# Kernel tuning notes

Measured on AMD Instinct MI355X. Metric: run time of the kernel, lower is better.

Reference implementation:

```python
import jax, jax.numpy as jnp
import numpy as np

NUM_BLOCKS = 8
WIDTH = 512
HIDDEN_SIZE_FACTOR = 1
HARD_THRESH_FRAC = 1.0
BLOCK_SIZE = WIDTH // NUM_BLOCKS


def setup_inputs() -> dict:
    key = jax.random.key(0)
    k_x, k1, k2, k3, k4 = jax.random.split(key, 5)
    B, L, P, C = 4, 2048, WIDTH, 8
    bs = BLOCK_SIZE
    hf = HIDDEN_SIZE_FACTOR
    scale = 1.0 / (bs * bs * hf)
    x = jax.random.normal(k_x, (B, L, P, C), dtype=jnp.float32)
    w1 = scale * jax.random.uniform(k1, (2, NUM_BLOCKS, bs, bs * hf), dtype=jnp.float32)
    b1 = scale * jax.random.uniform(k2, (2, NUM_BLOCKS, bs * hf), dtype=jnp.float32)
    w2 = scale * jax.random.uniform(k3, (2, NUM_BLOCKS, bs * hf, bs), dtype=jnp.float32)
    b2 = scale * jax.random.uniform(k4, (2, NUM_BLOCKS, bs), dtype=jnp.float32)
    return {"x": x, "w1": w1, "b1": b1, "w2": w2, "b2": b2}


def _gelu(v):
    # torch nn.GELU default is the exact (erf) variant
    return jax.nn.gelu(v, approximate=False)


def reference(x, w1, b1, w2, b2):
    B, L, P, C = x.shape
    nb, bs = NUM_BLOCKS, BLOCK_SIZE
    # rfft along L (norm='ortho'); complex64
    xf = jnp.fft.rfft(x, axis=1, norm="ortho")          # (B, Lf, P, C)
    Lf = xf.shape[1]
    xf = jnp.transpose(xf, (0, 1, 3, 2))                  # (B, Lf, C, P)
    xf = xf.reshape(B, Lf, C, nb, bs)                     # split P into blocks
    kept = int(Lf * HARD_THRESH_FRAC)
    xr, xi = jnp.real(xf[:, :kept]), jnp.imag(xf[:, :kept])
    # block-diagonal complex 2-layer MLP
    mm = lambda a, w: jnp.einsum("blcni,nio->blcno", a, w)
    o1r = _gelu(mm(xr, w1[0]) - mm(xi, w1[1]) + b1[0])
    o1i = _gelu(mm(xi, w1[0]) + mm(xr, w1[1]) + b1[1])
    o2r = mm(o1r, w2[0]) - mm(o1i, w2[1]) + b2[0]
    o2i = mm(o1i, w2[0]) + mm(o1r, w2[1]) + b2[1]
    # zero-pad the thresholded modes (no-op when kept == Lf)
    pad = Lf - kept
    if pad > 0:
        z = jnp.zeros((B, pad, C, nb, bs), dtype=o2r.dtype)
        o2r = jnp.concatenate([o2r, z], axis=1)
        o2i = jnp.concatenate([o2i, z], axis=1)
    xc = (o2r + 1j * o2i).reshape(B, Lf, C, P)
    out = jnp.fft.irfft(xc, n=L, axis=1, norm="ortho")  # (B, L, C, P)
    out = jnp.transpose(out, (0, 1, 3, 2))               # (B, L, P, C)
    return (out + x).astype(x.dtype)
```

## Files before the change

### kernel.cpp

```cpp
#include <hip/hip_runtime.h>
#include <hip/hip_bf16.h>

typedef unsigned short u16;
typedef unsigned int   u32;
typedef __bf16 bf16x8 __attribute__((ext_vector_type(8)));
typedef float  f32x4  __attribute__((ext_vector_type(4)));
typedef u32    u32x2  __attribute__((ext_vector_type(2)));

#define KPAD 1088
#define PI_F 3.14159265358979323846f

__device__ __forceinline__ u16 f2bf(float f){
    u32 u = __float_as_uint(f);
    return (u16)((u + 0x7FFFu + ((u >> 16) & 1u)) >> 16);
}
__device__ __forceinline__ float bf2f(u16 v){ return __uint_as_float(((u32)v) << 16); }
__device__ __forceinline__ int zmap(int e){ return e + (e >> 4); }
__device__ __forceinline__ int brev10(int x){ return (int)(__brev((u32)x) >> 22); }

__global__ __launch_bounds__(256) void prep_w(const float* __restrict__ w1,
                                              const float* __restrict__ w2,
                                              u16* __restrict__ WSW){
    int gid = blockIdx.x * 256 + threadIdx.x;
    int qd = gid >> 12;
    int t  = qd & 1;
    int n  = (qd >> 1) & 7;
    int l  = qd >> 4;
    int rr = gid & 4095;
    int o  = rr >> 6;
    int k  = rr & 63;
    const float* w = l ? w2 : w1;
    WSW[gid] = f2bf(w[((size_t)(t*8 + n)*64 + k)*64 + o]);
}


__device__ __forceinline__ u16 unpack_one(const float2* Zc, int k, int pl, float sf){
    int rb  = zmap(brev10(k & 1023));
    int rmb = zmap(brev10((1024 - k) & 1023));
    float2 Zk = Zc[rb], Zm = Zc[rmb];
    float sn_, cs_; __sincosf(PI_F*(float)k*(1.0f/1024.0f), &sn_, &cs_);
    float Er=0.5f*(Zk.x+Zm.x), Ei=0.5f*(Zk.y-Zm.y);
    float Dr=0.5f*(Zk.x-Zm.x), Di=0.5f*(Zk.y+Zm.y);
    float Xr = Er + cs_*Di - sn_*Dr;
    float Xi = Ei - sn_*Di - cs_*Dr;
    return f2bf((pl ? Xi : Xr) * sf);
}

__global__ __launch_bounds__(256) void fwd_fft(const float* __restrict__ X,
                                               u16* __restrict__ S){
    __shared__ float2 Zs[4*1088];
    __shared__ float2 tws[544];
    int tid = threadIdx.x;
    int blk = blockIdx.x;
    int b = blk >> 10;
    int q = blk & 1023;
    int m8 = q & 7, tq = q >> 3;
    int Q = (tq >> 2)*8 + m8, s4 = tq & 3;
    int col0 = Q*16 + s4*4;
    int p  = col0 >> 3;
    int c0 = col0 & 7;
    int n  = p >> 6, pl_ = p & 63;

    for (int i = tid; i < 512; i += 256){
        float sv, cv; __sincosf(-2.0f*PI_F*(float)i*(1.0f/1024.0f), &sv, &cv);
        tws[zmap(i)] = make_float2(cv, sv);
    }
    for (int pi = tid; pi < 1024; pi += 256){
        size_t base = ((size_t)(b*2048 + 2*pi)*512 + p)*8 + c0;
        f32x4 ve = *(const f32x4*)(X + base);
        f32x4 vo = *(const f32x4*)(X + base + 4096);
        #pragma unroll
        for (int s = 0; s < 4; ++s)
            Zs[s*1088 + zmap(pi)] = make_float2(ve[s], vo[s]);
    }
    __syncthreads();
    for (int ms = 9; ms >= 0; --ms){
        int m = 1 << ms;
        for (int i = tid; i < 2048; i += 256){
            int s = i >> 9, bi = i & 511;
            int jj = bi & (m-1);
            int a  = ((bi >> ms) << (ms+1)) + jj;
            float2 u = Zs[s*1088 + zmap(a)];
            float2 v = Zs[s*1088 + zmap(a+m)];
            float2 w = tws[zmap(jj << (9-ms))];
            float dx = u.x - v.x, dy = u.y - v.y;
            Zs[s*1088 + zmap(a)]   = make_float2(u.x+v.x, u.y+v.y);
            Zs[s*1088 + zmap(a+m)] = make_float2(dx*w.x - dy*w.y, dx*w.y + dy*w.x);
        }
        __syncthreads();
    }
    const float sf = 0.02209708691207961f;
    int run = tid >> 5, tr = tid & 31;
    int ci = run >> 1, pl = run & 1;
    const float2* Zc = Zs + ci*1088;
    u16* rp = S + (size_t)((((b*8 + (c0+ci))*8 + n)*2 + pl)*64 + pl_)*KPAD;
    for (int kk = tr*2; kk <= 1024; kk += 64){
        u16 w0 = unpack_one(Zc, kk, pl, sf);
        if (kk < 1024){
            u16 w1 = unpack_one(Zc, kk+1, pl, sf);
            *(u32*)(rp + kk) = (u32)w0 | ((u32)w1 << 16);
        } else {
            rp[kk] = w0;
        }
    }
}

__device__ __forceinline__ bf16x8 fetchB(const u16* mat, int o64, int k64, bool neg){
    const u32x2* pb = (const u32x2*)(mat + o64*68 + k64);
    u32x2 lo = pb[0], hi = pb[1];
    union { u32 u[4]; bf16x8 v; } bt;
    bt.u[0]=lo.x; bt.u[1]=lo.y; bt.u[2]=hi.x; bt.u[3]=hi.y;
    if (neg){ bt.u[0]^=0x80008000u; bt.u[1]^=0x80008000u; bt.u[2]^=0x80008000u; bt.u[3]^=0x80008000u; }
    return bt.v;
}
__device__ __forceinline__ bf16x8 loadU16x8(const u16* pp){
    union { u32 u[4]; bf16x8 v; } t;
    const u32* qq = (const u32*)pp;
    t.u[0]=qq[0]; t.u[1]=qq[1]; t.u[2]=qq[2]; t.u[3]=qq[3];
    return t.v;
}

__global__ __launch_bounds__(256) void mlp_kernel(const u16* __restrict__ WSW,
                                                  const float* __restrict__ b1,
                                                  const float* __restrict__ b2,
                                                  u16* __restrict__ S){
    __shared__ __align__(16) u16 AT[4][64*68];
    __shared__ __align__(16) u16 AS[8448];
    int tid = threadIdx.x;
    int blk = blockIdx.x;
    int n = blk & 7;
    int rest = blk >> 3;
    int t17 = rest % 17;
    int bc  = rest / 17;
    int b = bc >> 3, c = bc & 7;
    int k0 = t17 << 6;
    int lane = tid & 63, wv = tid >> 6;
    int lane15 = lane & 15, quad = lane >> 4;

    for (int mi = 0; mi < 4; ++mi){
        const u32* src = (const u32*)(WSW + (size_t)(((mi>>1)*8 + n)*2 + (mi&1))*4096);
        u32* dstm = (u32*)AT[mi];
        for (int d = tid; d < 2048; d += 256){
            int o = d >> 5, kk2 = d & 31;
            dstm[o*34 + kk2] = src[d];
        }
    }
    float bb1[8], bb2v[8];
    #pragma unroll
    for (int nb = 0; nb < 8; ++nb){
        int col = nb*16 + lane15;
        int tt = col >> 6, cc = col & 63;
        bb1[nb]  = b1[tt*512 + n*64 + cc];
        bb2v[nb] = b2[tt*512 + n*64 + cc];
    }
    size_t SB = (size_t)(((b*8 + c)*8 + n)*2)*64;
    {
        int rsub = tid & 31;
        for (int rr = tid >> 5; rr < 128; rr += 8){
            const u16* rp = S + (SB + rr)*KPAD + k0;
            u32 w = *(const u32*)(rp + 2*rsub);
            AS[(2*rsub)*132 + rr]   = (u16)(w & 0xFFFFu);
            AS[(2*rsub+1)*132 + rr] = (u16)(w >> 16);
        }
    }
    __syncthreads();

    const u16* arow = AS + (wv*16 + lane15)*132;
    bf16x8 afr[4];
    #pragma unroll
    for (int kb = 0; kb < 4; ++kb)
        afr[kb] = loadU16x8(arow + kb*32 + quad*8);
    f32x4 acc[8];
    #pragma unroll
    for (int nb = 0; nb < 8; ++nb){ acc[nb][0]=bb1[nb]; acc[nb][1]=bb1[nb]; acc[nb][2]=bb1[nb]; acc[nb][3]=bb1[nb]; }
    #pragma unroll
    for (int nb = 0; nb < 8; ++nb){
        int o64 = (nb&3)*16 + lane15;
        #pragma unroll
        for (int kb = 0; kb < 4; ++kb){
            int k64 = (kb&1)*32 + quad*8;
            const u16* mat; bool neg = false;
            if (kb < 2) mat = (nb<4) ? AT[0] : AT[1];
            else { if (nb<4){ mat = AT[1]; neg = true; } else mat = AT[0]; }
            acc[nb] = __builtin_amdgcn_mfma_f32_16x16x32_bf16(afr[kb], fetchB(mat,o64,k64,neg), acc[nb], 0,0,0);
        }
    }
    #pragma unroll
    for (int nb = 0; nb < 8; ++nb){
        #pragma unroll
        for (int r4 = 0; r4 < 4; ++r4){
            float xv = acc[nb][r4];
            float u_ = xv * 0.70710678118f;
            float u2 = u_*u_;
            float pg = 1.0f + u2*(-0.333333333f + u2*(0.1f + u2*(-0.0238095238f)));
            float h  = 0.5f * xv * (1.0f + 1.12837916709551f * u_ * pg);
            AS[(wv*16 + quad*4 + r4)*132 + nb*16 + lane15] = f2bf(h);
        }
    }
    bf16x8 a2[4];
    #pragma unroll
    for (int kb = 0; kb < 4; ++kb)
        a2[kb] = loadU16x8(arow + kb*32 + quad*8);
    f32x4 acc2[8];
    #pragma unroll
    for (int nb = 0; nb < 8; ++nb){ acc2[nb][0]=bb2v[nb]; acc2[nb][1]=bb2v[nb]; acc2[nb][2]=bb2v[nb]; acc2[nb][3]=bb2v[nb]; }
    #pragma unroll
    for (int nb = 0; nb < 8; ++nb){
        int o64 = (nb&3)*16 + lane15;
        #pragma unroll
        for (int kb = 0; kb < 4; ++kb){
            int k64 = (kb&1)*32 + quad*8;
            const u16* mat; bool neg = false;
            if (kb < 2) mat = (nb<4) ? AT[2] : AT[3];
            else { if (nb<4){ mat = AT[3]; neg = true; } else mat = AT[2]; }
            acc2[nb] = __builtin_amdgcn_mfma_f32_16x16x32_bf16(a2[kb], fetchB(mat,o64,k64,neg), acc2[nb], 0,0,0);
        }
    }
    __syncthreads();
    #pragma unroll
    for (int nb = 0; nb < 8; ++nb){
        #pragma unroll
        for (int r4 = 0; r4 < 4; ++r4)
            AS[(nb*16 + lane15)*66 + (wv*16 + quad*4 + r4)] = f2bf(acc2[nb][r4]);
    }
    __syncthreads();
    {
        int rsub = tid & 31;
        int k = k0 + 2*rsub;
        for (int rr = tid >> 5; rr < 128; rr += 8){
            u32 val = *(const u32*)(AS + rr*66 + 2*rsub);
            u16* rp = S + (SB + rr)*KPAD + k0;
            if (k + 1 <= 1024)  *(u32*)(rp + 2*rsub) = val;
            else if (k == 1024) rp[2*rsub] = (u16)(val & 0xFFFFu);
        }
    }
}

__global__ __launch_bounds__(256) void inv_fft(const u16* __restrict__ S,
                                               const float* __restrict__ X,
                                               float* __restrict__ OUT){
    __shared__ float2 Zs[4*1088];
    __shared__ float2 tws[544];
    __shared__ float2 ysp[4];
    int tid = threadIdx.x;
    int blk = blockIdx.x;
    int b = blk >> 10;
    int q = blk & 1023;
    int m8 = q & 7, tq = q >> 3;
    int Q = (tq >> 2)*8 + m8, s4 = tq & 3;
    int col0 = Q*16 + s4*4;
    int p  = col0 >> 3;
    int c0 = col0 & 7;
    int n  = p >> 6, pl_ = p & 63;

    for (int i = tid; i < 512; i += 256){
        float sv, cv; __sincosf(-2.0f*PI_F*(float)i*(1.0f/1024.0f), &sv, &cv);
        tws[zmap(i)] = make_float2(cv, sv);
    }
    {
        int g = tid >> 6, l64 = tid & 63;
        const u16* rpR = S + (size_t)((((b*8 + (c0+g))*8 + n)*2 + 0)*64 + pl_)*KPAD;
        const u16* rpI = rpR + (size_t)64*KPAD;
        for (int kk = 2*l64; kk <= 1024; kk += 128){
            u32 wr = *(const u32*)(rpR + kk);
            u32 wi = *(const u32*)(rpI + kk);
            float yr0 = bf2f((u16)(wr & 0xFFFFu));
            float yi0 = bf2f((u16)(wi & 0xFFFFu));
            if (kk == 0)        Zs[g*1088 + zmap(0)] = make_float2(yr0, 0.0f);
            else if (kk == 1024) ysp[g] = make_float2(yr0, 0.0f);
            else                Zs[g*1088 + zmap(kk)] = make_float2(yr0, yi0);
            if (kk < 1024){
                float yr1 = bf2f((u16)(wr >> 16));
                float yi1 = bf2f((u16)(wi >> 16));
                Zs[g*1088 + zmap(kk+1)] = make_float2(yr1, yi1);
            }
        }
    }
    __syncthreads();
    for (int k = tid; k <= 512; k += 256){
        float s2_, c2_; __sincosf(PI_F*(float)k*(1.0f/1024.0f), &s2_, &c2_);
        #pragma unroll
        for (int s = 0; s < 4; ++s){
            float2 Yk = Zs[s*1088 + zmap(k)];
            float2 Ym = (k == 0) ? ysp[s] : Zs[s*1088 + zmap(1024 - k)];
            float Ex = 0.5f*(Yk.x + Ym.x);
            float Ey = 0.5f*(Yk.y - Ym.y);
            float Dx = 0.5f*(Yk.x - Ym.x);
            float Dy = 0.5f*(Yk.y + Ym.y);
            float Ox = c2_*Dx - s2_*Dy;
            float Oy = c2_*Dy + s2_*Dx;
            Zs[s*1088 + zmap(k)] = make_float2(Ex - Oy, Ey + Ox);
            if (k > 0 && k < 512)
                Zs[s*1088 + zmap(1024 - k)] = make_float2(Ex + Oy, Ox - Ey);
        }
    }
    __syncthreads();
    for (int ms = 9; ms >= 0; --ms){
        int m = 1 << ms;
        for (int i = tid; i < 2048; i += 256){
            int s = i >> 9, bi = i & 511;
            int jj = bi & (m-1);
            int a  = ((bi >> ms) << (ms+1)) + jj;
            float2 u = Zs[s*1088 + zmap(a)];
            float2 v = Zs[s*1088 + zmap(a+m)];
            float2 w = tws[zmap(jj << (9-ms))];
            float dx = u.x - v.x, dy = u.y - v.y;
            Zs[s*1088 + zmap(a)]   = make_float2(u.x+v.x, u.y+v.y);
            Zs[s*1088 + zmap(a+m)] = make_float2(dx*w.x - dy*w.y, dx*w.y + dy*w.x);
        }
        __syncthreads();
    }
    const float sc = 0.04419417382415922f;
    for (int pi = tid; pi < 1024; pi += 256){
        int f = (1024 - pi) & 1023;
        int zb = zmap(brev10(f));
        size_t base = ((size_t)(b*2048 + 2*pi)*512 + p)*8 + c0;
        f32x4 xe = *(const f32x4*)(X + base);
        f32x4 xo = *(const f32x4*)(X + base + 4096);
        f32x4 oe, oo;
        #pragma unroll
        for (int s = 0; s < 4; ++s){
            float2 r = Zs[s*1088 + zb];
            oe[s] = r.x*sc + xe[s];
            oo[s] = r.y*sc + xo[s];
        }
        *(f32x4*)(OUT + base)        = oe;
        *(f32x4*)(OUT + base + 4096) = oo;
    }
}

extern "C" void kernel_launch(void* const* d_in, const int* in_sizes, int n_in,
                              void* d_out, int out_size, void* d_ws, size_t ws_size,
                              hipStream_t stream){
    (void)in_sizes; (void)n_in; (void)out_size; (void)ws_size;
    const float* x  = (const float*)d_in[0];
    const float* w1 = (const float*)d_in[1];
    const float* b1 = (const float*)d_in[2];
    const float* w2 = (const float*)d_in[3];
    const float* b2 = (const float*)d_in[4];
    float* out = (float*)d_out;
    u16* WSW = (u16*)d_ws;
    u16* S1  = (u16*)((char*)d_ws + (1 << 20));

    prep_w<<<dim3(512),  dim3(256), 0, stream>>>(w1, w2, WSW);
    fwd_fft<<<dim3(4096), dim3(256), 0, stream>>>(x, S1);
    mlp_kernel<<<dim3(4352), dim3(256), 0, stream>>>(WSW, b1, b2, S1);
    inv_fft<<<dim3(4096), dim3(256), 0, stream>>>(S1, x, out);
}
```

Before: 521.2 us.

## Replace radix-2 LDS FFT with radix-4/16 register FFT and batch MLP blocks

Replaces the 10-stage radix-2 shared-memory FFT (one barrier per stage, with a twiddle table) by a three-pass 4x16x16 decomposition. Each pass works on register arrays with twiddles computed on the fly, and the first forward pass runs straight from the global loads. The bit-reversed output index changes to a matching digit-permutation function. The MLP kernel now handles four (b,c) groups per block, so the weight tile loaded into LDS is reused across them, and the grid shrinks fourfold. The cost is higher register pressure in the FFT and more serial work per MLP block.

```diff
diff --git a/kernel.cpp b/kernel.cpp
--- a/kernel.cpp
+++ b/kernel.cpp
@@ -16,7 +16,94 @@
 }
 __device__ __forceinline__ float bf2f(u16 v){ return __uint_as_float(((u32)v) << 16); }
 __device__ __forceinline__ int zmap(int e){ return e + (e >> 4); }
-__device__ __forceinline__ int brev10(int x){ return (int)(__brev((u32)x) >> 22); }
+
+__device__ __forceinline__ int sig(int k){
+    k &= 1023;
+    int a = (k >> 6) + (((k >> 2) & 15) << 4) + ((k & 3) << 8);
+    return zmap(a);
+}
+
+__device__ __forceinline__ float2 cmul(float2 a, float2 b){
+    return make_float2(a.x*b.x - a.y*b.y, a.x*b.y + a.y*b.x);
+}
+__device__ __forceinline__ void fft4v(float2& x0, float2& x1, float2& x2, float2& x3){
+    float2 t0 = make_float2(x0.x+x2.x, x0.y+x2.y);
+    float2 t1 = make_float2(x0.x-x2.x, x0.y-x2.y);
+    float2 t2 = make_float2(x1.x+x3.x, x1.y+x3.y);
+    float2 t3 = make_float2(x1.x-x3.x, x1.y-x3.y);
+    x0 = make_float2(t0.x+t2.x, t0.y+t2.y);
+    x2 = make_float2(t0.x-t2.x, t0.y-t2.y);
+    x1 = make_float2(t1.x+t3.y, t1.y-t3.x);
+    x3 = make_float2(t1.x-t3.y, t1.y+t3.x);
+}
+__device__ __forceinline__ void fft16(float2 a[16]){
+    #pragma unroll
+    for (int u1 = 0; u1 < 4; ++u1) fft4v(a[u1], a[u1+4], a[u1+8], a[u1+12]);
+    const float Cq = 0.70710678118654752f;
+    const float c1 = 0.92387953251128674f, s1 = 0.38268343236508977f;
+    a[5]  = cmul(a[5],  make_float2(c1, -s1));
+    a[6]  = cmul(a[6],  make_float2(Cq, -Cq));
+    a[7]  = cmul(a[7],  make_float2(s1, -c1));
+    a[9]  = cmul(a[9],  make_float2(Cq, -Cq));
+    a[10] = cmul(a[10], make_float2(0.0f, -1.0f));
+    a[11] = cmul(a[11], make_float2(-Cq, -Cq));
+    a[13] = cmul(a[13], make_float2(s1, -c1));
+    a[14] = cmul(a[14], make_float2(-Cq, -Cq));
+    a[15] = cmul(a[15], make_float2(-c1, s1));
+    #pragma unroll
+    for (int ja = 0; ja < 4; ++ja) fft4v(a[4*ja], a[4*ja+1], a[4*ja+2], a[4*ja+3]);
+}
+
+__device__ __forceinline__ void fft_stepA_lds(float2* Zs, int tid){
+    int u = (tid >> 4) & 15;
+    float s_, c_;
+    __sincosf(-2.0f*PI_F*(float)u*(1.0f/64.0f), &s_, &c_);
+    float2 tw1 = make_float2(c_, s_);
+    float2 tw2 = cmul(tw1, tw1);
+    float2 tw3 = cmul(tw2, tw1);
+    #pragma unroll
+    for (int s = 0; s < 4; ++s){
+        float2* Z = Zs + s*1088;
+        float2 x0 = Z[zmap(tid)], x1 = Z[zmap(tid+256)], x2 = Z[zmap(tid+512)], x3 = Z[zmap(tid+768)];
+        fft4v(x0, x1, x2, x3);
+        Z[zmap(tid)]     = x0;
+        Z[zmap(tid+256)] = cmul(x1, tw1);
+        Z[zmap(tid+512)] = cmul(x2, tw2);
+        Z[zmap(tid+768)] = cmul(x3, tw3);
+    }
+}
+__device__ __forceinline__ void fft_stepB(float2* Zs, int tid){
+    int seq = tid >> 6, id = tid & 63;
+    int nA = id & 15, jv = id >> 4;
+    float2* Z = Zs + seq*1088;
+    float2 a[16];
+    #pragma unroll
+    for (int u = 0; u < 16; ++u) a[u] = Z[zmap(nA + 16*u + 256*jv)];
+    fft16(a);
+    float s_, c_;
+    __sincosf(-2.0f*PI_F*(float)(nA*jv)*(1.0f/1024.0f), &s_, &c_);
+    float2 tw = make_float2(c_, s_);
+    __sincosf(-2.0f*PI_F*(float)nA*(1.0f/256.0f), &s_, &c_);
+    float2 st = make_float2(c_, s_);
+    #pragma unroll
+    for (int ju = 0; ju < 16; ++ju){
+        float2 v = cmul(a[((ju&3)<<2)|(ju>>2)], tw);
+        Z[zmap(nA + 16*ju + 256*jv)] = v;
+        tw = cmul(tw, st);
+    }
+}
+__device__ __forceinline__ void fft_stepC(float2* Zs, int tid){
+    int seq = tid >> 6, kI = tid & 63;
+    int ju = kI >> 2, jv = kI & 3;
+    float2* Z = Zs + seq*1088;
+    float2 a[16];
+    #pragma unroll
+    for (int nA = 0; nA < 16; ++nA) a[nA] = Z[zmap(nA + 16*ju + 256*jv)];
+    fft16(a);
+    #pragma unroll
+    for (int kO = 0; kO < 16; ++kO)
+        Z[zmap(kO + 16*ju + 256*jv)] = a[((kO&3)<<2)|(kO>>2)];
+}
 
 __global__ __launch_bounds__(256) void prep_w(const float* __restrict__ w1,
                                               const float* __restrict__ w2,
@@ -35,9 +122,7 @@
 
 
 __device__ __forceinline__ u16 unpack_one(const float2* Zc, int k, int pl, float sf){
-    int rb  = zmap(brev10(k & 1023));
-    int rmb = zmap(brev10((1024 - k) & 1023));
-    float2 Zk = Zc[rb], Zm = Zc[rmb];
+    float2 Zk = Zc[sig(k)], Zm = Zc[sig(1024 - k)];
     float sn_, cs_; __sincosf(PI_F*(float)k*(1.0f/1024.0f), &sn_, &cs_);
     float Er=0.5f*(Zk.x+Zm.x), Ei=0.5f*(Zk.y-Zm.y);
     float Dr=0.5f*(Zk.x-Zm.x), Di=0.5f*(Zk.y+Zm.y);
@@ -49,7 +134,6 @@
 __global__ __launch_bounds__(256) void fwd_fft(const float* __restrict__ X,
                                                u16* __restrict__ S){
     __shared__ float2 Zs[4*1088];
-    __shared__ float2 tws[544];
     int tid = threadIdx.x;
     int blk = blockIdx.x;
     int b = blk >> 10;
@@ -61,34 +145,39 @@
     int c0 = col0 & 7;
     int n  = p >> 6, pl_ = p & 63;
 
-    for (int i = tid; i < 512; i += 256){
-        float sv, cv; __sincosf(-2.0f*PI_F*(float)i*(1.0f/1024.0f), &sv, &cv);
-        tws[zmap(i)] = make_float2(cv, sv);
-    }
-    for (int pi = tid; pi < 1024; pi += 256){
+    float2 zz[4][4];
+    #pragma unroll
+    for (int v = 0; v < 4; ++v){
+        int pi = tid + 256*v;
         size_t base = ((size_t)(b*2048 + 2*pi)*512 + p)*8 + c0;
         f32x4 ve = *(const f32x4*)(X + base);
         f32x4 vo = *(const f32x4*)(X + base + 4096);
         #pragma unroll
-        for (int s = 0; s < 4; ++s)
-            Zs[s*1088 + zmap(pi)] = make_float2(ve[s], vo[s]);
-    }
-    __syncthreads();
-    for (int ms = 9; ms >= 0; --ms){
-        int m = 1 << ms;
-        for (int i = tid; i < 2048; i += 256){
-            int s = i >> 9, bi = i & 511;
-            int jj = bi & (m-1);
-            int a  = ((bi >> ms) << (ms+1)) + jj;
-            float2 u = Zs[s*1088 + zmap(a)];
-            float2 v = Zs[s*1088 + zmap(a+m)];
-            float2 w = tws[zmap(jj << (9-ms))];
-            float dx = u.x - v.x, dy = u.y - v.y;
-            Zs[s*1088 + zmap(a)]   = make_float2(u.x+v.x, u.y+v.y);
-            Zs[s*1088 + zmap(a+m)] = make_float2(dx*w.x - dy*w.y, dx*w.y + dy*w.x);
-        }
-        __syncthreads();
-    }
+        for (int s = 0; s < 4; ++s) zz[v][s] = make_float2(ve[s], vo[s]);
+    }
+    {
+        int u = (tid >> 4) & 15;
+        float s_, c_;
+        __sincosf(-2.0f*PI_F*(float)u*(1.0f/64.0f), &s_, &c_);
+        float2 tw1 = make_float2(c_, s_);
+        float2 tw2 = cmul(tw1, tw1);
+        float2 tw3 = cmul(tw2, tw1);
+        #pragma unroll
+        for (int s = 0; s < 4; ++s){
+            float2 x0 = zz[0][s], x1 = zz[1][s], x2 = zz[2][s], x3 = zz[3][s];
+            fft4v(x0, x1, x2, x3);
+            float2* Z = Zs + s*1088;
+            Z[zmap(tid)]     = x0;
+            Z[zmap(tid+256)] = cmul(x1, tw1);
+            Z[zmap(tid+512)] = cmul(x2, tw2);
+            Z[zmap(tid+768)] = cmul(x3, tw3);
+        }
+    }
+    __syncthreads();
+    fft_stepB(Zs, tid);
+    __syncthreads();
+    fft_stepC(Zs, tid);
+    __syncthreads();
     const float sf = 0.02209708691207961f;
     int run = tid >> 5, tr = tid & 31;
     int ci = run >> 1, pl = run & 1;
@@ -131,8 +220,7 @@
     int n = blk & 7;
     int rest = blk >> 3;
     int t17 = rest % 17;
-    int bc  = rest / 17;
-    int b = bc >> 3, c = bc & 7;
+    int bcg = rest / 17;
     int k0 = t17 << 6;
     int lane = tid & 63, wv = tid >> 6;
     int lane15 = lane & 15, quad = lane >> 4;
@@ -153,86 +241,92 @@
         bb1[nb]  = b1[tt*512 + n*64 + cc];
         bb2v[nb] = b2[tt*512 + n*64 + cc];
     }
-    size_t SB = (size_t)(((b*8 + c)*8 + n)*2)*64;
-    {
-        int rsub = tid & 31;
-        for (int rr = tid >> 5; rr < 128; rr += 8){
-            const u16* rp = S + (SB + rr)*KPAD + k0;
-            u32 w = *(const u32*)(rp + 2*rsub);
-            AS[(2*rsub)*132 + rr]   = (u16)(w & 0xFFFFu);
-            AS[(2*rsub+1)*132 + rr] = (u16)(w >> 16);
-        }
-    }
-    __syncthreads();
-
-    const u16* arow = AS + (wv*16 + lane15)*132;
-    bf16x8 afr[4];
-    #pragma unroll
-    for (int kb = 0; kb < 4; ++kb)
-        afr[kb] = loadU16x8(arow + kb*32 + quad*8);
-    f32x4 acc[8];
-    #pragma unroll
-    for (int nb = 0; nb < 8; ++nb){ acc[nb][0]=bb1[nb]; acc[nb][1]=bb1[nb]; acc[nb][2]=bb1[nb]; acc[nb][3]=bb1[nb]; }
-    #pragma unroll
-    for (int nb = 0; nb < 8; ++nb){
-        int o64 = (nb&3)*16 + lane15;
-        #pragma unroll
-        for (int kb = 0; kb < 4; ++kb){
-            int k64 = (kb&1)*32 + quad*8;
-            const u16* mat; bool neg = false;
-            if (kb < 2) mat = (nb<4) ? AT[0] : AT[1];
-            else { if (nb<4){ mat = AT[1]; neg = true; } else mat = AT[0]; }
-            acc[nb] = __builtin_amdgcn_mfma_f32_16x16x32_bf16(afr[kb], fetchB(mat,o64,k64,neg), acc[nb], 0,0,0);
-        }
-    }
-    #pragma unroll
-    for (int nb = 0; nb < 8; ++nb){
-        #pragma unroll
-        for (int r4 = 0; r4 < 4; ++r4){
-            float xv = acc[nb][r4];
-            float u_ = xv * 0.70710678118f;
-            float u2 = u_*u_;
-            float pg = 1.0f + u2*(-0.333333333f + u2*(0.1f + u2*(-0.0238095238f)));
-            float h  = 0.5f * xv * (1.0f + 1.12837916709551f * u_ * pg);
-            AS[(wv*16 + quad*4 + r4)*132 + nb*16 + lane15] = f2bf(h);
-        }
-    }
-    bf16x8 a2[4];
-    #pragma unroll
-    for (int kb = 0; kb < 4; ++kb)
-        a2[kb] = loadU16x8(arow + kb*32 + quad*8);
-    f32x4 acc2[8];
-    #pragma unroll
-    for (int nb = 0; nb < 8; ++nb){ acc2[nb][0]=bb2v[nb]; acc2[nb][1]=bb2v[nb]; acc2[nb][2]=bb2v[nb]; acc2[nb][3]=bb2v[nb]; }
-    #pragma unroll
-    for (int nb = 0; nb < 8; ++nb){
-        int o64 = (nb&3)*16 + lane15;
-        #pragma unroll
-        for (int kb = 0; kb < 4; ++kb){
-            int k64 = (kb&1)*32 + quad*8;
-            const u16* mat; bool neg = false;
-            if (kb < 2) mat = (nb<4) ? AT[2] : AT[3];
-            else { if (nb<4){ mat = AT[3]; neg = true; } else mat = AT[2]; }
-            acc2[nb] = __builtin_amdgcn_mfma_f32_16x16x32_bf16(a2[kb], fetchB(mat,o64,k64,neg), acc2[nb], 0,0,0);
-        }
-    }
-    __syncthreads();
-    #pragma unroll
-    for (int nb = 0; nb < 8; ++nb){
-        #pragma unroll
-        for (int r4 = 0; r4 < 4; ++r4)
-            AS[(nb*16 + lane15)*66 + (wv*16 + quad*4 + r4)] = f2bf(acc2[nb][r4]);
-    }
-    __syncthreads();
-    {
-        int rsub = tid & 31;
-        int k = k0 + 2*rsub;
-        for (int rr = tid >> 5; rr < 128; rr += 8){
-            u32 val = *(const u32*)(AS + rr*66 + 2*rsub);
-            u16* rp = S + (SB + rr)*KPAD + k0;
-            if (k + 1 <= 1024)  *(u32*)(rp + 2*rsub) = val;
-            else if (k == 1024) rp[2*rsub] = (u16)(val & 0xFFFFu);
-        }
+    __syncthreads();
+
+    for (int it = 0; it < 4; ++it){
+        int bc = bcg*4 + it;
+        int b = bc >> 3, c = bc & 7;
+        size_t SB = (size_t)(((b*8 + c)*8 + n)*2)*64;
+        {
+            int rsub = tid & 31;
+            for (int rr = tid >> 5; rr < 128; rr += 8){
+                const u16* rp = S + (SB + rr)*KPAD + k0;
+                u32 w = *(const u32*)(rp + 2*rsub);
+                AS[(2*rsub)*132 + rr]   = (u16)(w & 0xFFFFu);
+                AS[(2*rsub+1)*132 + rr] = (u16)(w >> 16);
+            }
+        }
+        __syncthreads();
+        const u16* arow = AS + (wv*16 + lane15)*132;
+        bf16x8 afr[4];
+        #pragma unroll
+        for (int kb = 0; kb < 4; ++kb)
+            afr[kb] = loadU16x8(arow + kb*32 + quad*8);
+        f32x4 acc[8];
+        #pragma unroll
+        for (int nb = 0; nb < 8; ++nb){ acc[nb][0]=bb1[nb]; acc[nb][1]=bb1[nb]; acc[nb][2]=bb1[nb]; acc[nb][3]=bb1[nb]; }
+        #pragma unroll
+        for (int nb = 0; nb < 8; ++nb){
+            int o64 = (nb&3)*16 + lane15;
+            #pragma unroll
+            for (int kb = 0; kb < 4; ++kb){
+                int k64 = (kb&1)*32 + quad*8;
+                const u16* mat; bool neg = false;
+                if (kb < 2) mat = (nb<4) ? AT[0] : AT[1];
+                else { if (nb<4){ mat = AT[1]; neg = true; } else mat = AT[0]; }
+                acc[nb] = __builtin_amdgcn_mfma_f32_16x16x32_bf16(afr[kb], fetchB(mat,o64,k64,neg), acc[nb], 0,0,0);
+            }
+        }
+        #pragma unroll
+        for (int nb = 0; nb < 8; ++nb){
+            #pragma unroll
+            for (int r4 = 0; r4 < 4; ++r4){
+                float xv = acc[nb][r4];
+                float u_ = xv * 0.70710678118f;
+                float u2 = u_*u_;
+                float pg = 1.0f + u2*(-0.333333333f + u2*(0.1f + u2*(-0.0238095238f)));
+                float h  = 0.5f * xv * (1.0f + 1.12837916709551f * u_ * pg);
+                AS[(wv*16 + quad*4 + r4)*132 + nb*16 + lane15] = f2bf(h);
+            }
+        }
+        bf16x8 a2[4];
+        #pragma unroll
+        for (int kb = 0; kb < 4; ++kb)
+            a2[kb] = loadU16x8(arow + kb*32 + quad*8);
+        f32x4 acc2[8];
+        #pragma unroll
+        for (int nb = 0; nb < 8; ++nb){ acc2[nb][0]=bb2v[nb]; acc2[nb][1]=bb2v[nb]; acc2[nb][2]=bb2v[nb]; acc2[nb][3]=bb2v[nb]; }
+        #pragma unroll
+        for (int nb = 0; nb < 8; ++nb){
+            int o64 = (nb&3)*16 + lane15;
+            #pragma unroll
+            for (int kb = 0; kb < 4; ++kb){
+                int k64 = (kb&1)*32 + quad*8;
+                const u16* mat; bool neg = false;
+                if (kb < 2) mat = (nb<4) ? AT[2] : AT[3];
+                else { if (nb<4){ mat = AT[3]; neg = true; } else mat = AT[2]; }
+                acc2[nb] = __builtin_amdgcn_mfma_f32_16x16x32_bf16(a2[kb], fetchB(mat,o64,k64,neg), acc2[nb], 0,0,0);
+            }
+        }
+        __syncthreads();
+        #pragma unroll
+        for (int nb = 0; nb < 8; ++nb){
+            #pragma unroll
+            for (int r4 = 0; r4 < 4; ++r4)
+                AS[(nb*16 + lane15)*66 + (wv*16 + quad*4 + r4)] = f2bf(acc2[nb][r4]);
+        }
+        __syncthreads();
+        {
+            int rsub = tid & 31;
+            int k = k0 + 2*rsub;
+            for (int rr = tid >> 5; rr < 128; rr += 8){
+                u32 val = *(const u32*)(AS + rr*66 + 2*rsub);
+                u16* rp = S + (SB + rr)*KPAD + k0;
+                if (k + 1 <= 1024)  *(u32*)(rp + 2*rsub) = val;
+                else if (k == 1024) rp[2*rsub] = (u16)(val & 0xFFFFu);
+            }
+        }
+        __syncthreads();
     }
 }
 
@@ -240,7 +334,6 @@
                                                const float* __restrict__ X,
                                                float* __restrict__ OUT){
     __shared__ float2 Zs[4*1088];
-    __shared__ float2 tws[544];
     __shared__ float2 ysp[4];
     int tid = threadIdx.x;
     int blk = blockIdx.x;
@@ -253,10 +346,6 @@
     int c0 = col0 & 7;
     int n  = p >> 6, pl_ = p & 63;
 
-    for (int i = tid; i < 512; i += 256){
-        float sv, cv; __sincosf(-2.0f*PI_F*(float)i*(1.0f/1024.0f), &sv, &cv);
-        tws[zmap(i)] = make_float2(cv, sv);
-    }
     {
         int g = tid >> 6, l64 = tid & 63;
         const u16* rpR = S + (size_t)((((b*8 + (c0+g))*8 + n)*2 + 0)*64 + pl_)*KPAD;
@@ -266,9 +355,9 @@
             u32 wi = *(const u32*)(rpI + kk);
             float yr0 = bf2f((u16)(wr & 0xFFFFu));
             float yi0 = bf2f((u16)(wi & 0xFFFFu));
-            if (kk == 0)        Zs[g*1088 + zmap(0)] = make_float2(yr0, 0.0f);
+            if (kk == 0)         Zs[g*1088 + zmap(0)] = make_float2(yr0, 0.0f);
             else if (kk == 1024) ysp[g] = make_float2(yr0, 0.0f);
-            else                Zs[g*1088 + zmap(kk)] = make_float2(yr0, yi0);
+            else                 Zs[g*1088 + zmap(kk)] = make_float2(yr0, yi0);
             if (kk < 1024){
                 float yr1 = bf2f((u16)(wr >> 16));
                 float yi1 = bf2f((u16)(wi >> 16));
@@ -295,25 +384,15 @@
         }
     }
     __syncthreads();
-    for (int ms = 9; ms >= 0; --ms){
-        int m = 1 << ms;
-        for (int i = tid; i < 2048; i += 256){
-            int s = i >> 9, bi = i & 511;
-            int jj = bi & (m-1);
-            int a  = ((bi >> ms) << (ms+1)) + jj;
-            float2 u = Zs[s*1088 + zmap(a)];
-            float2 v = Zs[s*1088 + zmap(a+m)];
-            float2 w = tws[zmap(jj << (9-ms))];
-            float dx = u.x - v.x, dy = u.y - v.y;
-            Zs[s*1088 + zmap(a)]   = make_float2(u.x+v.x, u.y+v.y);
-            Zs[s*1088 + zmap(a+m)] = make_float2(dx*w.x - dy*w.y, dx*w.y + dy*w.x);
-        }
-        __syncthreads();
-    }
+    fft_stepA_lds(Zs, tid);
+    __syncthreads();
+    fft_stepB(Zs, tid);
+    __syncthreads();
+    fft_stepC(Zs, tid);
+    __syncthreads();
     const float sc = 0.04419417382415922f;
     for (int pi = tid; pi < 1024; pi += 256){
-        int f = (1024 - pi) & 1023;
-        int zb = zmap(brev10(f));
+        int zb = sig(1024 - pi);
         size_t base = ((size_t)(b*2048 + 2*pi)*512 + p)*8 + c0;
         f32x4 xe = *(const f32x4*)(X + base);
         f32x4 xo = *(const f32x4*)(X + base + 4096);
@@ -344,6 +423,6 @@
 
     prep_w<<<dim3(512),  dim3(256), 0, stream>>>(w1, w2, WSW);
     fwd_fft<<<dim3(4096), dim3(256), 0, stream>>>(x, S1);
-    mlp_kernel<<<dim3(4352), dim3(256), 0, stream>>>(WSW, b1, b2, S1);
+    mlp_kernel<<<dim3(1088), dim3(256), 0, stream>>>(WSW, b1, b2, S1);
     inv_fft<<<dim3(4096), dim3(256), 0, stream>>>(S1, x, out);
 }
```

Result: no change. 530.7 us (+1.8%).
